# Kernel optimization log

Measured on AMD Instinct MI355X. Metric: run time of the kernel, lower is better.

Reference implementation:

```python
import jax, jax.numpy as jnp
import numpy as np

MODEL_DIM = 1024
HEAD_SIZE = 128

def setup_inputs() -> dict:
    key = jax.random.key(0)
    k0, k1, k2, k3 = jax.random.split(key, 4)
    embedded = jax.random.normal(k0, (4, 4096, MODEL_DIM), dtype=jnp.float32)
    # nn.Linear(model_dim, head_size, bias=False) weights: [head_size, model_dim]
    s = 1.0 / np.sqrt(MODEL_DIM)
    Wk = jax.random.uniform(k1, (HEAD_SIZE, MODEL_DIM), jnp.float32, -s, s)
    Wq = jax.random.uniform(k2, (HEAD_SIZE, MODEL_DIM), jnp.float32, -s, s)
    Wv = jax.random.uniform(k3, (HEAD_SIZE, MODEL_DIM), jnp.float32, -s, s)
    return {"embedded": embedded, "Wk": Wk, "Wq": Wq, "Wv": Wv}

def reference(embedded, Wk, Wq, Wv):
    # embedded: [b, s, m]; W*: [h, m]
    keys = jnp.einsum('bsm,hm->bsh', embedded, Wk)
    queries = jnp.einsum('bsm,hm->bsh', embedded, Wq)
    values = jnp.einsum('bsm,hm->bsh', embedded, Wv)
    h = keys.shape[-1]
    scores = jnp.einsum('bqh,bkh->bqk', queries, keys) / jnp.sqrt(jnp.float32(h))  # [b,s,s]
    s_len = keys.shape[1]
    causal = jnp.tril(jnp.ones((s_len, s_len), dtype=bool))
    scores = jnp.where(causal, scores, -jnp.inf)
    probs = jax.nn.softmax(scores, axis=-1)
    return jnp.einsum('bqk,bkh->bqh', probs, values)
```

## Files before the change

### kernel.cpp

```cpp
#include <hip/hip_runtime.h>
#include <hip/hip_bf16.h>


#define SEQ 4096
#define BATCH 4
#define HS 128
#define SLOTS_PB 128

typedef unsigned short u16;
typedef __bf16 bf16x8 __attribute__((ext_vector_type(8)));
typedef _Float16 f16x4 __attribute__((ext_vector_type(4)));
typedef float f32x4 __attribute__((ext_vector_type(4)));

__device__ __forceinline__ u16 f2bf(float f) {
    union { float f; unsigned u; } v; v.f = f;
    unsigned u = v.u;
    return (u16)((u + 0x7FFFu + ((u >> 16) & 1u)) >> 16);
}
__device__ __forceinline__ float bf2f(u16 u) {
    union { unsigned u; float f; } v; v.u = ((unsigned)u) << 16; return v.f;
}
__device__ __forceinline__ u16 f2h(float f) {
    union { _Float16 h; u16 u; } v; v.h = (_Float16)f; return v.u;
}
__device__ __forceinline__ void async_cp16(const void* g, void* l) {
    __builtin_amdgcn_global_load_lds(
        (const __attribute__((address_space(1))) unsigned int*)g,
        (__attribute__((address_space(3))) unsigned int*)l, 16, 0, 0);
}
__device__ __forceinline__ int nsplit_of(int Q) {
    return Q / 5 + 1 + (Q >= 23 ? 1 : 0);
}

__global__ __launch_bounds__(256) void wconv_kernel(
    const float* __restrict__ Wk, const float* __restrict__ Wq,
    const float* __restrict__ Wv, u16* __restrict__ Wt)
{
    const int g    = blockIdx.x * 256 + threadIdx.x;
    const int lane = g & 63;
    const int kf   = (g >> 6) & 1;
    const int kc   = (g >> 7) & 15;
    const int nt   = g >> 11;
    const int row  = nt * 16 + (lane & 15);
    const int k0   = kc * 64 + kf * 32 + (lane >> 4) * 8;
    const float* src = (row < 128) ? Wk : ((row < 256) ? Wq : Wv);
    const float scale = (row >= 128 && row < 256)
        ? 0.08838834764831845f * 1.4426950408889634f : 1.0f;
    const float4 v0 = *(const float4*)&src[(size_t)(row & 127) * 1024 + k0];
    const float4 v1 = *(const float4*)&src[(size_t)(row & 127) * 1024 + k0 + 4];
    ushort4 a, b;
    a.x = f2bf(v0.x * scale); a.y = f2bf(v0.y * scale);
    a.z = f2bf(v0.z * scale); a.w = f2bf(v0.w * scale);
    b.x = f2bf(v1.x * scale); b.y = f2bf(v1.y * scale);
    b.z = f2bf(v1.z * scale); b.w = f2bf(v1.w * scale);
    *(ushort4*)&Wt[(size_t)g * 8]     = a;
    *(ushort4*)&Wt[(size_t)g * 8 + 4] = b;
}

__global__ __launch_bounds__(256, 2) void qkv_kernel(
    const float* __restrict__ emb, const u16* __restrict__ Wt,
    u16* __restrict__ Qf, u16* __restrict__ Kf, u16* __restrict__ Vf)
{
    __shared__ u16 sE[2][32][72];
    __shared__ u16 sOut[32][392];

    const int tid  = threadIdx.x;
    const int wv   = tid >> 6;
    const int lane = tid & 63;
    const int quad = lane >> 4;
    const int l16  = lane & 15;
    const int R0   = blockIdx.x * 32;

    const int arow = tid >> 3, ac8 = tid & 7;
    const float* abase = &emb[(size_t)(R0 + arow) * 1024 + ac8 * 8];

    f32x4 acc[2][6];
    #pragma unroll
    for (int rg = 0; rg < 2; rg++)
        #pragma unroll
        for (int nt = 0; nt < 6; nt++) acc[rg][nt] = (f32x4){0.f, 0.f, 0.f, 0.f};

    bf16x8 B0[12], B1[12];

#define LOADB(kci, B)                                                          \
    {                                                                          \
        _Pragma("unroll")                                                      \
        for (int nt = 0; nt < 6; nt++) {                                       \
            const size_t g = ((size_t)((wv * 6 + nt) * 16 + (kci)) * 2) * 64 + lane; \
            B[2 * nt]     = *(const bf16x8*)&Wt[g * 8];                        \
            B[2 * nt + 1] = *(const bf16x8*)&Wt[(g + 64) * 8];                 \
        }                                                                      \
    }
#define WRITEA(buf, v0, v1)                                                    \
    {                                                                          \
        ushort4 lo, hi;                                                        \
        lo.x = f2bf((v0).x); lo.y = f2bf((v0).y);                              \
        lo.z = f2bf((v0).z); lo.w = f2bf((v0).w);                              \
        hi.x = f2bf((v1).x); hi.y = f2bf((v1).y);                              \
        hi.z = f2bf((v1).z); hi.w = f2bf((v1).w);                              \
        *(ushort4*)&sE[buf][arow][ac8 * 8]     = lo;                           \
        *(ushort4*)&sE[buf][arow][ac8 * 8 + 4] = hi;                           \
    }
#define COMPUTE(buf, B)                                                        \
    {                                                                          \
        bf16x8 a[2][2];                                                        \
        _Pragma("unroll")                                                      \
        for (int rg = 0; rg < 2; rg++)                                         \
            _Pragma("unroll")                                                  \
            for (int kf = 0; kf < 2; kf++)                                     \
                a[rg][kf] = *(const bf16x8*)&sE[buf][rg * 16 + l16][kf * 32 + quad * 8]; \
        _Pragma("unroll")                                                      \
        for (int nt = 0; nt < 6; nt++)                                         \
            _Pragma("unroll")                                                  \
            for (int rg = 0; rg < 2; rg++) {                                   \
                acc[rg][nt] = __builtin_amdgcn_mfma_f32_16x16x32_bf16(a[rg][0], B[2 * nt],     acc[rg][nt], 0, 0, 0); \
                acc[rg][nt] = __builtin_amdgcn_mfma_f32_16x16x32_bf16(a[rg][1], B[2 * nt + 1], acc[rg][nt], 0, 0, 0); \
            }                                                                  \
    }

    float4 av0 = *(const float4*)&abase[0];
    float4 av1 = *(const float4*)&abase[4];
    LOADB(0, B0);
    WRITEA(0, av0, av1);

    for (int it = 0; it < 8; it++) {
        const int k1 = 2 * it + 1;
        __syncthreads();
        av0 = *(const float4*)&abase[k1 * 64];
        av1 = *(const float4*)&abase[k1 * 64 + 4];
        LOADB(k1, B1);
        COMPUTE(0, B0);
        WRITEA(1, av0, av1);
        __syncthreads();
        if (it < 7) {
            av0 = *(const float4*)&abase[(k1 + 1) * 64];
            av1 = *(const float4*)&abase[(k1 + 1) * 64 + 4];
            LOADB(k1 + 1, B0);
        }
        COMPUTE(1, B1);
        if (it < 7) WRITEA(0, av0, av1);
    }

    #pragma unroll
    for (int nt = 0; nt < 6; nt++) {
        const int col = wv * 96 + nt * 16 + l16;
        #pragma unroll
        for (int rg = 0; rg < 2; rg++) {
            const int rl = rg * 16 + quad * 4;
            #pragma unroll
            for (int r = 0; r < 4; r++) {
                const float v = acc[rg][nt][r];
                sOut[rl + r][col] = (col < 256) ? f2bf(v) : f2h(v);
            }
        }
    }
    __syncthreads();

    const int b  = R0 >> 12;
    const int s0 = R0 & 4095;
    #pragma unroll
    for (int i = 0; i < 2; i++) {
        const int g    = tid + i * 256;
        const int lg   = g & 63;
        const int kfp  = (g >> 6) & 3;
        const int k16l = g >> 8;
        const int rl   = k16l * 16 + (lg & 15);
        const int cl   = kfp * 32 + (lg >> 4) * 8;
        const size_t base = (((size_t)(b * 256 + (s0 >> 4) + k16l) * 4 + kfp) * 64 + lg) * 8;
        *(uint4*)&Kf[base] = *(const uint4*)&sOut[rl][cl];
        *(uint4*)&Qf[base] = *(const uint4*)&sOut[rl][128 + cl];
    }
    #pragma unroll
    for (int i = 0; i < 4; i++) {
        const int g   = tid + i * 256;
        const int lg  = g & 63;
        const int ntl = (g >> 6) & 1;
        const int ht  = g >> 7;
        const int h   = ht * 16 + (lg & 15);
        const int kl  = ntl * 16 + ((lg >> 4) & 3) * 4;
        ushort4 o;
        o.x = sOut[kl + 0][256 + h];
        o.y = sOut[kl + 1][256 + h];
        o.z = sOut[kl + 2][256 + h];
        o.w = sOut[kl + 3][256 + h];
        const int t64 = s0 >> 6;
        const int ntg = ((s0 >> 4) & 3) + ntl;
        const size_t base = ((((size_t)(b * 64 + t64) * 8 + ht) * 4 + ntg) * 64 + lg) * 4;
        *(ushort4*)&Vf[base] = o;
    }
#undef LOADB
#undef WRITEA
#undef COMPUTE
}

template<bool DIRECT>
__global__ __launch_bounds__(512, 4) void attn_kernel(
    const u16* __restrict__ Qf, const u16* __restrict__ Kf,
    const u16* __restrict__ Vf, u16* __restrict__ Opart,
    float* __restrict__ lpart, float* __restrict__ out)
{
    __shared__ u16 sT[3][8192];

    const int tid  = threadIdx.x;
    const int wv   = tid >> 6;
    const int lane = tid & 63;
    const int quad = lane >> 4;
    const int l16  = lane & 15;

    const int L    = blockIdx.x;
    const int b    = L & 3;
    const int slot = L >> 2;

    int Q = 0, sp = 0;
    if constexpr (DIRECT) {
        Q = slot; sp = 0;
    } else {
        int acc = 0;
        #pragma unroll 1
        for (int qq = 0; qq < 32; ++qq) {
            const int n = nsplit_of(qq);
            if (slot < acc + n) { Q = qq; sp = slot - acc; break; }
            acc += n;
        }
    }
    const int total = 4 * Q + 4;
    const int ns    = DIRECT ? 1 : nsplit_of(Q);
    const int kbeg  = DIRECT ? 0 : (sp * total) / ns;
    const int kend  = DIRECT ? total : ((sp + 1) * total) / ns;

    const int q0 = Q * 128;
    const size_t bS = (size_t)b * SEQ;

    const char* KbB = (const char*)(Kf + (size_t)b * 524288);
    const char* VbB = (const char*)(Vf + (size_t)b * 524288);

    bf16x8 qf[4];
    const int q16 = Q * 8 + wv;
    #pragma unroll
    for (int kf = 0; kf < 4; kf++)
        qf[kf] = *(const bf16x8*)&Qf[(((size_t)(b * 256 + q16) * 4 + kf) * 64 + lane) * 8];

    float rs0 = 0.f;
    f32x4 O[8];
    #pragma unroll
    for (int ht = 0; ht < 8; ht++) O[ht] = (f32x4){0.f, 0.f, 0.f, 0.f};

    const int qg0 = q0 + wv * 16 + l16;

#define STAGE(bufi, kt)                                                        \
    {                                                                          \
        async_cp16(KbB + (size_t)(kt) * 8192 + wv * 1024 + lane * 16,          \
                   (char*)&sT[bufi][0] + wv * 1024);                           \
        async_cp16(VbB + ((((size_t)((kt) >> 1) * 8 + wv) * 4 + ((kt) & 1) * 2) << 9) + lane * 16, \
                   (char*)&sT[bufi][4096] + wv * 1024);                        \
    }
#define WAITBAR(N)                                                             \
    {                                                                          \
        asm volatile("s_waitcnt vmcnt(" #N ")" ::: "memory");                  \
        __builtin_amdgcn_sched_barrier(0);                                     \
        __builtin_amdgcn_s_barrier();                                          \
        __builtin_amdgcn_sched_barrier(0);                                     \
    }

    STAGE(0, kbeg);
    STAGE(1, kbeg + 1);
    WAITBAR(2);

    int bcur = 0;
    for (int kt = kbeg; kt < kend; ++kt) {
        const bool more = (kt + 2 < kend);
        if (more) {
            const int b2 = (bcur >= 1) ? bcur - 1 : bcur + 2;
            STAGE(b2, kt + 2);
        }

        const bool diag = (kt >= 4 * Q);
        f16x4 pf0[2];
        #pragma unroll
        for (int nt = 0; nt < 2; nt++) {
            f32x4 s0 = (f32x4){0.f, 0.f, 0.f, 0.f};
            __builtin_amdgcn_s_setprio(1);
            #pragma unroll
            for (int kf = 0; kf < 4; kf++) {
                const bf16x8 kfr = *(const bf16x8*)&sT[bcur][((nt * 4 + kf) << 9) + lane * 8];
                s0 = __builtin_amdgcn_mfma_f32_16x16x32_bf16(kfr, qf[kf], s0, 0, 0, 0);
            }
            __builtin_amdgcn_s_setprio(0);
            if (diag) {
                #pragma unroll
                for (int r = 0; r < 4; r++) {
                    const int kg = kt * 32 + nt * 16 + quad * 4 + r;
                    if (kg > qg0) s0[r] = -3.0e38f;
                }
            }
            f16x4 p0;
            #pragma unroll
            for (int r = 0; r < 4; r++) {
                const float e0 = exp2f(s0[r] - 4.0f);
                rs0 += e0;
                p0[r] = (_Float16)e0;
            }
            pf0[nt] = p0;
        }

        __builtin_amdgcn_s_setprio(1);
        #pragma unroll
        for (int ht = 0; ht < 8; ht++) {
            f16x4 vf[2];
            #pragma unroll
            for (int nt = 0; nt < 2; nt++)
                vf[nt] = *(const f16x4*)&sT[bcur][4096 + ((ht * 2 + nt) << 8) + lane * 4];
            #pragma unroll
            for (int nt = 0; nt < 2; nt++)
                O[ht] = __builtin_amdgcn_mfma_f32_16x16x16f16(vf[nt], pf0[nt], O[ht], 0, 0, 0);
        }
        __builtin_amdgcn_s_setprio(0);

        if (more) { WAITBAR(2); } else { WAITBAR(0); }
        bcur = (bcur == 2) ? 0 : bcur + 1;
    }
#undef STAGE
#undef WAITBAR

    rs0 += __shfl_xor(rs0, 16); rs0 += __shfl_xor(rs0, 32);

    if constexpr (DIRECT) {
        const float inv = 1.0f / rs0;
        const int q = q0 + wv * 16 + l16;
        #pragma unroll
        for (int ht = 0; ht < 8; ht++) {
            f32x4 o = O[ht] * inv;
            *(f32x4*)&out[(bS + q) * HS + ht * 16 + quad * 4] = o;
        }
    } else {
        const size_t slotbase = (size_t)b * SLOTS_PB + slot;
        #pragma unroll
        for (int ht = 0; ht < 8; ht++) {
            const size_t j = ((slotbase * 8 + wv) * 8 + ht) * 64 + lane;
            ushort4 o;
            o.x = f2bf(O[ht][0]); o.y = f2bf(O[ht][1]);
            o.z = f2bf(O[ht][2]); o.w = f2bf(O[ht][3]);
            *(ushort4*)&Opart[j * 4] = o;
        }
        if (quad == 0)
            lpart[slotbase * 128 + wv * 16 + l16] = rs0;
    }
}

__global__ __launch_bounds__(256) void merge_kernel(
    const u16* __restrict__ Opart, const float* __restrict__ lpart,
    float* __restrict__ out)
{
    const int g    = blockIdx.x * 256 + threadIdx.x;
    const int lane = g & 63;
    const int ht   = (g >> 6) & 7;
    const int wvv  = (g >> 9) & 7;
    const int Q    = (g >> 12) & 31;
    const int b    = g >> 17;
    const int l16  = lane & 15;
    const int qd   = lane >> 4;

    int pre = 0, ns = 0;
    #pragma unroll 1
    for (int qq = 0; qq < 32; ++qq) {
        const int n = nsplit_of(qq);
        if (qq < Q) pre += n;
        else if (qq == Q) { ns = n; break; }
    }
    const size_t base_slot = (size_t)b * SLOTS_PB + pre;
    const int ql = wvv * 16 + l16;

    float den = 0.f;
    f32x4 num = (f32x4){0.f, 0.f, 0.f, 0.f};
    #pragma unroll 1
    for (int s = 0; s < ns; s++) {
        den += lpart[(base_slot + s) * 128 + ql];
        const size_t j = (((base_slot + s) * 8 + wvv) * 8 + ht) * 64 + lane;
        const ushort4 o = *(const ushort4*)&Opart[j * 4];
        num[0] += bf2f(o.x); num[1] += bf2f(o.y);
        num[2] += bf2f(o.z); num[3] += bf2f(o.w);
    }
    const float inv = 1.0f / den;
    float4 o; o.x = num[0] * inv; o.y = num[1] * inv;
    o.z = num[2] * inv; o.w = num[3] * inv;
    const size_t off = ((size_t)b << 19) +
                       (size_t)(Q * 128 + wvv * 16 + l16) * 128 +
                       (size_t)(ht * 4 + qd) * 4;
    *(float4*)&out[off] = o;
}

extern "C" void kernel_launch(void* const* d_in, const int* in_sizes, int n_in,
                              void* d_out, int out_size, void* d_ws, size_t ws_size,
                              hipStream_t stream) {
    const float* emb = (const float*)d_in[0];
    const float* Wk  = (const float*)d_in[1];
    const float* Wq  = (const float*)d_in[2];
    const float* Wv  = (const float*)d_in[3];
    float* out = (float*)d_out;

    char* ws = (char*)d_ws;
    const size_t WBF_SZ    = (size_t)384 * 1024 * 2;
    const size_t QKV_SZ    = (size_t)BATCH * SEQ * HS * 2;
    const size_t Q_OFF     = WBF_SZ;
    const size_t K_OFF     = Q_OFF + QKV_SZ;
    const size_t V_OFF     = K_OFF + QKV_SZ;
    const size_t OPART_OFF = V_OFF + QKV_SZ;
    const size_t OPART_SZ  = (size_t)BATCH * SLOTS_PB * 32768;
    const size_t L_SZ      = (size_t)BATCH * SLOTS_PB * 128 * 4;

    u16* Wt = (u16*)ws;
    u16* Qf = (u16*)(ws + Q_OFF);
    u16* Kf = (u16*)(ws + K_OFF);
    u16* Vf = (u16*)(ws + V_OFF);

    wconv_kernel<<<dim3(192), dim3(256), 0, stream>>>(Wk, Wq, Wv, Wt);
    qkv_kernel<<<dim3(512), dim3(256), 0, stream>>>(emb, Wt, Qf, Kf, Vf);

    const size_t need = OPART_OFF + OPART_SZ + L_SZ;

    if (ws_size >= need) {
        u16*   Opart = (u16*)(ws + OPART_OFF);
        float* lp    = (float*)(ws + OPART_OFF + OPART_SZ);
        attn_kernel<false><<<dim3(4 * SLOTS_PB), dim3(512), 0, stream>>>(Qf, Kf, Vf, Opart, lp, out);
        merge_kernel<<<dim3(BATCH * SEQ * HS / 4 / 256), dim3(256), 0, stream>>>(Opart, lp, out);
    } else {
        attn_kernel<true><<<dim3(32 * BATCH), dim3(512), 0, stream>>>(Qf, Kf, Vf, nullptr, nullptr, out);
    }
}
```

Before: 159.5 us.

## Double query tile per block to 256 rows, reuse K/V tiles across two query groups

Each attention block now covers 256 query rows instead of 128, with every wave holding two 16-row query groups that share each staged K/V tile. The split-K scheduling moves to a new per-double-tile split table, and waves skip KV tiles lying entirely above their causal diagonal. The goal is to halve K/V global-to-LDS traffic per query and add MFMA work per LDS load. In exchange, register pressure rises (two sets of O accumulators), and waves sit idle on fully masked tiles while still joining the block barriers. Partial outputs double in size and the merge kernel indexing changes to match.

```diff
diff --git a/kernel.cpp b/kernel.cpp
--- a/kernel.cpp
+++ b/kernel.cpp
@@ -28,8 +28,8 @@
         (const __attribute__((address_space(1))) unsigned int*)g,
         (__attribute__((address_space(3))) unsigned int*)l, 16, 0, 0);
 }
-__device__ __forceinline__ int nsplit_of(int Q) {
-    return Q / 5 + 1 + (Q >= 23 ? 1 : 0);
+__device__ __forceinline__ int nsplit2_of(int Q2) {
+    return (Q2 < 8) ? (Q2 + 1) : Q2;
 }
 
 __global__ __launch_bounds__(256) void wconv_kernel(
@@ -208,44 +208,50 @@
     const int l16  = lane & 15;
 
     const int L    = blockIdx.x;
-    const int b    = L & 3;
+    const int b    = DIRECT ? (L & 3) : (L & 3);
     const int slot = L >> 2;
 
-    int Q = 0, sp = 0;
+    int Q2 = 0, sp = 0;
     if constexpr (DIRECT) {
-        Q = slot; sp = 0;
+        Q2 = slot; sp = 0;
     } else {
         int acc = 0;
         #pragma unroll 1
-        for (int qq = 0; qq < 32; ++qq) {
-            const int n = nsplit_of(qq);
-            if (slot < acc + n) { Q = qq; sp = slot - acc; break; }
+        for (int qq = 0; qq < 16; ++qq) {
+            const int n = nsplit2_of(qq);
+            if (slot < acc + n) { Q2 = qq; sp = slot - acc; break; }
             acc += n;
         }
     }
-    const int total = 4 * Q + 4;
-    const int ns    = DIRECT ? 1 : nsplit_of(Q);
+    const int total = 8 * Q2 + 8;
+    const int ns    = DIRECT ? 1 : nsplit2_of(Q2);
     const int kbeg  = DIRECT ? 0 : (sp * total) / ns;
     const int kend  = DIRECT ? total : ((sp + 1) * total) / ns;
 
-    const int q0 = Q * 128;
+    const int q0 = Q2 * 256;
     const size_t bS = (size_t)b * SEQ;
 
     const char* KbB = (const char*)(Kf + (size_t)b * 524288);
     const char* VbB = (const char*)(Vf + (size_t)b * 524288);
 
-    bf16x8 qf[4];
-    const int q16 = Q * 8 + wv;
-    #pragma unroll
-    for (int kf = 0; kf < 4; kf++)
-        qf[kf] = *(const bf16x8*)&Qf[(((size_t)(b * 256 + q16) * 4 + kf) * 64 + lane) * 8];
-
-    float rs0 = 0.f;
-    f32x4 O[8];
-    #pragma unroll
-    for (int ht = 0; ht < 8; ht++) O[ht] = (f32x4){0.f, 0.f, 0.f, 0.f};
-
-    const int qg0 = q0 + wv * 16 + l16;
+    bf16x8 qf[2][4];
+    #pragma unroll
+    for (int qg = 0; qg < 2; qg++) {
+        const int q16 = Q2 * 16 + wv * 2 + qg;
+        #pragma unroll
+        for (int kf = 0; kf < 4; kf++)
+            qf[qg][kf] = *(const bf16x8*)&Qf[(((size_t)(b * 256 + q16) * 4 + kf) * 64 + lane) * 8];
+    }
+
+    float rs0 = 0.f, rs1 = 0.f;
+    f32x4 O[2][8];
+    #pragma unroll
+    for (int qg = 0; qg < 2; qg++)
+        #pragma unroll
+        for (int ht = 0; ht < 8; ht++) O[qg][ht] = (f32x4){0.f, 0.f, 0.f, 0.f};
+
+    const int qg0 = q0 + wv * 32 + l16;
+    const int D   = 8 * Q2 + wv;
 
 #define STAGE(bufi, kt)                                                        \
     {                                                                          \
@@ -274,47 +280,55 @@
             STAGE(b2, kt + 2);
         }
 
-        const bool diag = (kt >= 4 * Q);
-        f16x4 pf0[2];
-        #pragma unroll
-        for (int nt = 0; nt < 2; nt++) {
-            f32x4 s0 = (f32x4){0.f, 0.f, 0.f, 0.f};
+        if (kt <= D) {
+            const bool diag = (kt == D);
+            f16x4 pf0[2], pf1[2];
+            #pragma unroll
+            for (int nt = 0; nt < 2; nt++) {
+                f32x4 s0 = (f32x4){0.f, 0.f, 0.f, 0.f};
+                f32x4 s1 = (f32x4){0.f, 0.f, 0.f, 0.f};
+                __builtin_amdgcn_s_setprio(1);
+                #pragma unroll
+                for (int kf = 0; kf < 4; kf++) {
+                    const bf16x8 kfr = *(const bf16x8*)&sT[bcur][((nt * 4 + kf) << 9) + lane * 8];
+                    s0 = __builtin_amdgcn_mfma_f32_16x16x32_bf16(kfr, qf[0][kf], s0, 0, 0, 0);
+                    s1 = __builtin_amdgcn_mfma_f32_16x16x32_bf16(kfr, qf[1][kf], s1, 0, 0, 0);
+                }
+                __builtin_amdgcn_s_setprio(0);
+                if (diag) {
+                    #pragma unroll
+                    for (int r = 0; r < 4; r++) {
+                        const int kg = kt * 32 + nt * 16 + quad * 4 + r;
+                        if (kg > qg0)      s0[r] = -3.0e38f;
+                        if (kg > qg0 + 16) s1[r] = -3.0e38f;
+                    }
+                }
+                f16x4 p0, p1;
+                #pragma unroll
+                for (int r = 0; r < 4; r++) {
+                    const float e0 = exp2f(s0[r] - 4.0f);
+                    const float e1 = exp2f(s1[r] - 4.0f);
+                    rs0 += e0; rs1 += e1;
+                    p0[r] = (_Float16)e0; p1[r] = (_Float16)e1;
+                }
+                pf0[nt] = p0; pf1[nt] = p1;
+            }
+
             __builtin_amdgcn_s_setprio(1);
             #pragma unroll
-            for (int kf = 0; kf < 4; kf++) {
-                const bf16x8 kfr = *(const bf16x8*)&sT[bcur][((nt * 4 + kf) << 9) + lane * 8];
-                s0 = __builtin_amdgcn_mfma_f32_16x16x32_bf16(kfr, qf[kf], s0, 0, 0, 0);
+            for (int ht = 0; ht < 8; ht++) {
+                f16x4 vf[2];
+                #pragma unroll
+                for (int nt = 0; nt < 2; nt++)
+                    vf[nt] = *(const f16x4*)&sT[bcur][4096 + ((ht * 2 + nt) << 8) + lane * 4];
+                #pragma unroll
+                for (int nt = 0; nt < 2; nt++) {
+                    O[0][ht] = __builtin_amdgcn_mfma_f32_16x16x16f16(vf[nt], pf0[nt], O[0][ht], 0, 0, 0);
+                    O[1][ht] = __builtin_amdgcn_mfma_f32_16x16x16f16(vf[nt], pf1[nt], O[1][ht], 0, 0, 0);
+                }
             }
             __builtin_amdgcn_s_setprio(0);
-            if (diag) {
-                #pragma unroll
-                for (int r = 0; r < 4; r++) {
-                    const int kg = kt * 32 + nt * 16 + quad * 4 + r;
-                    if (kg > qg0) s0[r] = -3.0e38f;
-                }
-            }
-            f16x4 p0;
-            #pragma unroll
-            for (int r = 0; r < 4; r++) {
-                const float e0 = exp2f(s0[r] - 4.0f);
-                rs0 += e0;
-                p0[r] = (_Float16)e0;
-            }
-            pf0[nt] = p0;
-        }
-
-        __builtin_amdgcn_s_setprio(1);
-        #pragma unroll
-        for (int ht = 0; ht < 8; ht++) {
-            f16x4 vf[2];
-            #pragma unroll
-            for (int nt = 0; nt < 2; nt++)
-                vf[nt] = *(const f16x4*)&sT[bcur][4096 + ((ht * 2 + nt) << 8) + lane * 4];
-            #pragma unroll
-            for (int nt = 0; nt < 2; nt++)
-                O[ht] = __builtin_amdgcn_mfma_f32_16x16x16f16(vf[nt], pf0[nt], O[ht], 0, 0, 0);
-        }
-        __builtin_amdgcn_s_setprio(0);
+        }
 
         if (more) { WAITBAR(2); } else { WAITBAR(0); }
         bcur = (bcur == 2) ? 0 : bcur + 1;
@@ -323,27 +337,35 @@
 #undef WAITBAR
 
     rs0 += __shfl_xor(rs0, 16); rs0 += __shfl_xor(rs0, 32);
+    rs1 += __shfl_xor(rs1, 16); rs1 += __shfl_xor(rs1, 32);
 
     if constexpr (DIRECT) {
-        const float inv = 1.0f / rs0;
-        const int q = q0 + wv * 16 + l16;
-        #pragma unroll
-        for (int ht = 0; ht < 8; ht++) {
-            f32x4 o = O[ht] * inv;
-            *(f32x4*)&out[(bS + q) * HS + ht * 16 + quad * 4] = o;
+        #pragma unroll
+        for (int qg = 0; qg < 2; qg++) {
+            const float inv = 1.0f / (qg ? rs1 : rs0);
+            const int q = q0 + wv * 32 + qg * 16 + l16;
+            #pragma unroll
+            for (int ht = 0; ht < 8; ht++) {
+                f32x4 o = O[qg][ht] * inv;
+                *(f32x4*)&out[(bS + q) * HS + ht * 16 + quad * 4] = o;
+            }
         }
     } else {
         const size_t slotbase = (size_t)b * SLOTS_PB + slot;
         #pragma unroll
-        for (int ht = 0; ht < 8; ht++) {
-            const size_t j = ((slotbase * 8 + wv) * 8 + ht) * 64 + lane;
-            ushort4 o;
-            o.x = f2bf(O[ht][0]); o.y = f2bf(O[ht][1]);
-            o.z = f2bf(O[ht][2]); o.w = f2bf(O[ht][3]);
-            *(ushort4*)&Opart[j * 4] = o;
-        }
-        if (quad == 0)
-            lpart[slotbase * 128 + wv * 16 + l16] = rs0;
+        for (int qg = 0; qg < 2; qg++)
+            #pragma unroll
+            for (int ht = 0; ht < 8; ht++) {
+                const size_t j = (((slotbase * 8 + wv) * 2 + qg) * 8 + ht) * 64 + lane;
+                ushort4 o;
+                o.x = f2bf(O[qg][ht][0]); o.y = f2bf(O[qg][ht][1]);
+                o.z = f2bf(O[qg][ht][2]); o.w = f2bf(O[qg][ht][3]);
+                *(ushort4*)&Opart[j * 4] = o;
+            }
+        if (quad == 0) {
+            lpart[slotbase * 256 + wv * 32 + l16]      = rs0;
+            lpart[slotbase * 256 + wv * 32 + 16 + l16] = rs1;
+        }
     }
 }
 
@@ -354,28 +376,29 @@
     const int g    = blockIdx.x * 256 + threadIdx.x;
     const int lane = g & 63;
     const int ht   = (g >> 6) & 7;
-    const int wvv  = (g >> 9) & 7;
-    const int Q    = (g >> 12) & 31;
+    const int qg   = (g >> 9) & 1;
+    const int wvv  = (g >> 10) & 7;
+    const int Q2   = (g >> 13) & 15;
     const int b    = g >> 17;
     const int l16  = lane & 15;
     const int qd   = lane >> 4;
 
     int pre = 0, ns = 0;
     #pragma unroll 1
-    for (int qq = 0; qq < 32; ++qq) {
-        const int n = nsplit_of(qq);
-        if (qq < Q) pre += n;
-        else if (qq == Q) { ns = n; break; }
+    for (int qq = 0; qq < 16; ++qq) {
+        const int n = nsplit2_of(qq);
+        if (qq < Q2) pre += n;
+        else if (qq == Q2) { ns = n; break; }
     }
     const size_t base_slot = (size_t)b * SLOTS_PB + pre;
-    const int ql = wvv * 16 + l16;
+    const int ql = wvv * 32 + qg * 16 + l16;
 
     float den = 0.f;
     f32x4 num = (f32x4){0.f, 0.f, 0.f, 0.f};
     #pragma unroll 1
     for (int s = 0; s < ns; s++) {
-        den += lpart[(base_slot + s) * 128 + ql];
-        const size_t j = (((base_slot + s) * 8 + wvv) * 8 + ht) * 64 + lane;
+        den += lpart[(base_slot + s) * 256 + ql];
+        const size_t j = ((((base_slot + s) * 8 + wvv) * 2 + qg) * 8 + ht) * 64 + lane;
         const ushort4 o = *(const ushort4*)&Opart[j * 4];
         num[0] += bf2f(o.x); num[1] += bf2f(o.y);
         num[2] += bf2f(o.z); num[3] += bf2f(o.w);
@@ -384,7 +407,7 @@
     float4 o; o.x = num[0] * inv; o.y = num[1] * inv;
     o.z = num[2] * inv; o.w = num[3] * inv;
     const size_t off = ((size_t)b << 19) +
-                       (size_t)(Q * 128 + wvv * 16 + l16) * 128 +
+                       (size_t)(Q2 * 256 + wvv * 32 + qg * 16 + l16) * 128 +
                        (size_t)(ht * 4 + qd) * 4;
     *(float4*)&out[off] = o;
 }
@@ -405,8 +428,8 @@
     const size_t K_OFF     = Q_OFF + QKV_SZ;
     const size_t V_OFF     = K_OFF + QKV_SZ;
     const size_t OPART_OFF = V_OFF + QKV_SZ;
-    const size_t OPART_SZ  = (size_t)BATCH * SLOTS_PB * 32768;
-    const size_t L_SZ      = (size_t)BATCH * SLOTS_PB * 128 * 4;
+    const size_t OPART_SZ  = (size_t)BATCH * SLOTS_PB * 65536;
+    const size_t L_SZ      = (size_t)BATCH * SLOTS_PB * 256 * 4;
 
     u16* Wt = (u16*)ws;
     u16* Qf = (u16*)(ws + Q_OFF);
@@ -424,6 +447,6 @@
         attn_kernel<false><<<dim3(4 * SLOTS_PB), dim3(512), 0, stream>>>(Qf, Kf, Vf, Opart, lp, out);
         merge_kernel<<<dim3(BATCH * SEQ * HS / 4 / 256), dim3(256), 0, stream>>>(Opart, lp, out);
     } else {
-        attn_kernel<true><<<dim3(32 * BATCH), dim3(512), 0, stream>>>(Qf, Kf, Vf, nullptr, nullptr, out);
-    }
-}
+        attn_kernel<true><<<dim3(16 * BATCH), dim3(512), 0, stream>>>(Qf, Kf, Vf, nullptr, nullptr, out);
+    }
+}
```

Result: slower. 183.6 us (+15.1%).
